# Optimization experiments

Measured on AMD Instinct MI355X. Metric: run time of the kernel, lower is better.

## Reference

```python
import jax, jax.numpy as jnp
import numpy as np

B = 16          # batch
DF = 1536       # dinov2 feature dim
D = 1024        # projected dim (32*32)
V = 6890        # SMPL vertices (hard-coded in DECO)
PD = 256        # vertex positional-embedding dim
HID = 512       # feature_transform hidden dim
C = 133         # semantic contact classes


def setup_inputs() -> dict:
    key = jax.random.key(0)
    ks = jax.random.split(key, 16)
    s = 0.02
    n = lambda k, shp: s * jax.random.normal(k, shp, dtype=jnp.float32)
    return {
        "features": jax.random.normal(ks[0], (B, DF), dtype=jnp.float32),
        "W_scene": n(ks[1], (DF, D)), "b_scene": jnp.zeros((D,), jnp.float32),
        "W_contact": n(ks[2], (DF, D)), "b_contact": jnp.zeros((D,), jnp.float32),
        "Wq": n(ks[3], (D, D)), "Wk": n(ks[4], (D, D)),
        "Wv": n(ks[5], (D, D)), "Wo": n(ks[6], (D, D)),
        "W_cls": n(ks[7], (D, V)), "b_cls": jnp.zeros((V,), jnp.float32),
        "pos_emb": n(ks[8], (V, PD)),
        "W_ft1": n(ks[9], (D + PD, HID)), "b_ft1": jnp.zeros((HID,), jnp.float32),
        "W_ft2": n(ks[10], (HID, C)), "b_ft2": jnp.zeros((C,), jnp.float32),
    }


def reference(features, W_scene, b_scene, W_contact, b_contact,
              Wq, Wk, Wv, Wo, W_cls, b_cls, pos_emb,
              W_ft1, b_ft1, W_ft2, b_ft2):
    b = features.shape[0]
    # projectors (dinov2 branch)
    sem = features @ W_scene + b_scene          # [B, D]
    part = features @ W_contact + b_contact     # [B, D]
    # cross attention over seq-len-1 tokens: q from sem, k/v from part
    q = (sem @ Wq)[:, None, :]                  # [B, 1, D]
    k = (part @ Wk)[:, None, :]
    v = (part @ Wv)[:, None, :]
    scores = jnp.einsum('bqd,bkd->bqk', q, k) / jnp.sqrt(jnp.float32(D))
    w = jax.nn.softmax(scores, axis=-1)
    att = jnp.einsum('bqk,bkd->bqd', w, v) @ Wo  # [B, 1, D]
    # per-vertex contact probability
    cont = jax.nn.sigmoid(att[:, 0, :] @ W_cls + b_cls)  # [B, V]
    # shared semantic classifier: the torch code loops over batches, does
    # nonzero() on (cont > 0.5), gathers pos embeddings for contact vertices,
    # runs feature_transform, and scatters into zeros(B, C, V). The masked
    # vectorized form below computes identical values.
    mask = cont > 0.5                           # [B, V] (int constant wrt grad)
    att_bv = jnp.broadcast_to(att, (b, V, D))   # att[b] repeated per vertex
    pos_bv = jnp.broadcast_to(pos_emb[None], (b, V, PD))
    combined = jnp.concatenate([att_bv, pos_bv], axis=-1)   # [B, V, D+PD]
    h = jax.nn.relu(combined @ W_ft1 + b_ft1)   # [B, V, HID]
    preds = h @ W_ft2 + b_ft2                   # [B, V, C]
    semantic_cont = jnp.where(mask[:, None, :],
                              jnp.transpose(preds, (0, 2, 1)),
                              jnp.float32(0.0))  # [B, C, V]
    return (cont, semantic_cont)
```

## Files before the change

kernel.cpp:

```cpp
#include <hip/hip_runtime.h>
#include <hip/hip_bf16.h>

#define B_   16
#define DF_  1536
#define D_   1024
#define V_   6890
#define PD_  256
#define HID_ 512
#define C_   133
#define VPAD 6912
#define CPAD 144

typedef short short8 __attribute__((ext_vector_type(8)));
typedef float float4_ __attribute__((ext_vector_type(4)));
typedef unsigned short ushort_t;

#define MFMA16 __builtin_amdgcn_mfma_f32_16x16x32_bf16

__device__ __forceinline__ float b2f(ushort_t u) {
  union { unsigned int i; float f; } x;
  x.i = ((unsigned int)u) << 16;
  return x.f;
}
__device__ __forceinline__ ushort_t f2b(float f) {
  union { float f; unsigned int i; } x;
  x.f = f;
  unsigned int r = (x.i + 0x7fffu + ((x.i >> 16) & 1u)) >> 16;
  return (ushort_t)r;
}
__device__ __forceinline__ unsigned int f22u(float h0, float h1) {
  __hip_bfloat162 hb = __float22bfloat162_rn(make_float2(h0, h1));
  unsigned int u;
  __builtin_memcpy(&u, &hb, sizeof(u));
  return u;
}

__global__ __launch_bounds__(256) void k_gemv_fA(const float* __restrict__ A,
                                                 const float* __restrict__ W,
                                                 const float* __restrict__ bias,
                                                 double* __restrict__ outd,
                                                 float* __restrict__ outf,
                                                 int K, int N) {
  int jl = threadIdx.x & 15, ks = threadIdx.x >> 4;
  int b  = blockIdx.y;
  int j  = blockIdx.x * 16 + jl;
  int klen = K >> 4;
  const float* Ar = A + b * K + ks * klen;
  const float* Wp = W + (size_t)(ks * klen) * N + j;
  double acc = 0.0;
#pragma unroll 8
  for (int kk = 0; kk < klen; ++kk)
    acc += (double)Ar[kk] * (double)Wp[(size_t)kk * N];
  __shared__ double red[16][16];
  red[ks][jl] = acc;
  __syncthreads();
  if (threadIdx.x < 16) {
    int jj = blockIdx.x * 16 + threadIdx.x;
    double s = 0.0;
#pragma unroll
    for (int q = 0; q < 16; ++q) s += red[q][threadIdx.x];
    if (bias) s += (double)bias[jj];
    if (outd) outd[b * N + jj] = s;
    if (outf) outf[b * N + jj] = (float)s;
  }
}

__global__ __launch_bounds__(256) void k_gemv_dA(const double* __restrict__ A,
                                                 const float* __restrict__ W,
                                                 const float* __restrict__ bias,
                                                 double* __restrict__ outd,
                                                 float* __restrict__ outf,
                                                 int K, int N) {
  int jl = threadIdx.x & 15, ks = threadIdx.x >> 4;
  int b  = blockIdx.y;
  int j  = blockIdx.x * 16 + jl;
  int klen = K >> 4;
  const double* Ar = A + b * K + ks * klen;
  const float*  Wp = W + (size_t)(ks * klen) * N + j;
  double acc = 0.0;
#pragma unroll 8
  for (int kk = 0; kk < klen; ++kk)
    acc += Ar[kk] * (double)Wp[(size_t)kk * N];
  __shared__ double red[16][16];
  red[ks][jl] = acc;
  __syncthreads();
  if (threadIdx.x < 16) {
    int jj = blockIdx.x * 16 + threadIdx.x;
    double s = 0.0;
#pragma unroll
    for (int q = 0; q < 16; ++q) s += red[q][threadIdx.x];
    if (bias) s += (double)bias[jj];
    if (outd) outd[b * N + jj] = s;
    if (outf) outf[b * N + jj] = (float)s;
  }
}

__global__ __launch_bounds__(256) void k_cont(const double* __restrict__ att,
                                              const float* __restrict__ Wcls,
                                              const float* __restrict__ bcls,
                                              unsigned char* __restrict__ maskb,
                                              float* __restrict__ out0) {
  int vl = threadIdx.x & 15, ks = threadIdx.x >> 4;
  int v  = blockIdx.x * 16 + vl;
  int vc = v < V_ ? v : V_ - 1;
  double acc[B_];
#pragma unroll
  for (int b = 0; b < B_; ++b) acc[b] = 0.0;
  int k0 = ks * 64;
  for (int kk = 0; kk < 64; ++kk) {
    int k = k0 + kk;
    double w = (double)Wcls[(size_t)k * V_ + vc];
#pragma unroll
    for (int b = 0; b < B_; ++b) acc[b] += att[b * D_ + k] * w;
  }
  __shared__ double red[16][B_][16];
#pragma unroll
  for (int b = 0; b < B_; ++b) red[ks][b][vl] = acc[b];
  __syncthreads();
  int b = threadIdx.x >> 4;
  double s = 0.0;
#pragma unroll
  for (int q = 0; q < 16; ++q) s += red[q][b][vl];
  if (v < V_) {
    s += (double)bcls[v];
    maskb[b * V_ + v] = (s > 0.0) ? 1 : 0;
    out0[b * V_ + v] = (float)(1.0 / (1.0 + exp(-s)));
  }
}

__global__ __launch_bounds__(256) void k_prep(const float* __restrict__ Wft2,
                                              const float* __restrict__ Wft1,
                                              ushort_t* __restrict__ WT,
                                              ushort_t* __restrict__ WbT) {
  int i = blockIdx.x * 256 + threadIdx.x;
  if (i < CPAD * HID_) {
    int c = i >> 9, k = i & (HID_ - 1);
    WT[i] = (c < C_) ? f2b(Wft2[(size_t)k * C_ + c]) : (ushort_t)0;
  } else {
    int j = i - CPAD * HID_;
    if (j < HID_ * PD_) {
      int k = j & (HID_ - 1), pd = j >> 9;
      WbT[(size_t)k * PD_ + pd] = f2b(Wft1[(size_t)(D_ + pd) * HID_ + k]);
    }
  }
}

#define LDSROW 264
__global__ __launch_bounds__(256) void k_pproj(const float* __restrict__ pos,
                                               const ushort_t* __restrict__ WbT,
                                               ushort_t* __restrict__ PP) {
  __shared__ ushort_t sp[64 * LDSROW];
  int v0 = blockIdx.x * 64;
#pragma unroll
  for (int k = 0; k < 16; ++k) {
    int flat4 = k * 256 + threadIdx.x;
    int row = flat4 >> 6, col4 = flat4 & 63;
    int vr = v0 + row; vr = vr < V_ ? vr : V_ - 1;
    float4_ x = *(const float4_*)(pos + (size_t)vr * PD_ + col4 * 4);
    unsigned int* dst = (unsigned int*)&sp[row * LDSROW + col4 * 4];
    dst[0] = f22u(x[0], x[1]);
    dst[1] = f22u(x[2], x[3]);
  }
  __syncthreads();

  int wave = threadIdx.x >> 6, lane = threadIdx.x & 63;
  int q = lane >> 4, l15 = lane & 15;
  int n0 = blockIdx.y * 64;
  float4_ acc[4] = {};
  for (int kt = 0; kt < 8; ++kt) {
    int jb = kt * 32 + q * 8;
    short8 a = *(const short8*)&sp[(wave * 16 + l15) * LDSROW + jb];
#pragma unroll
    for (int nf = 0; nf < 4; ++nf) {
      int n = n0 + nf * 16 + l15;
      short8 bfr = *(const short8*)(WbT + (size_t)n * PD_ + jb);
      acc[nf] = MFMA16(a, bfr, acc[nf], 0, 0, 0);
    }
  }
  int v0w = v0 + wave * 16 + q * 4;
#pragma unroll
  for (int nf = 0; nf < 4; ++nf)
#pragma unroll
    for (int r = 0; r < 4; ++r)
      PP[(size_t)(v0w + r) * HID_ + (n0 + nf * 16 + l15)] = f2b(acc[nf][r]);
}

__global__ __launch_bounds__(256, 2) void k_main(const ushort_t* __restrict__ WT,
                                                 const ushort_t* __restrict__ PP,
                                                 const float* __restrict__ attproj,
                                                 const unsigned char* __restrict__ maskb,
                                                 const float* __restrict__ bft2,
                                                 float* __restrict__ out1) {
  int b0 = blockIdx.y * 2;
  int wave = threadIdx.x >> 6, lane = threadIdx.x & 63;
  int q = lane >> 4, l15 = lane & 15;
  int vbase = blockIdx.x * 128 + wave * 32;

  __shared__ float attp[2][HID_];
  for (int i = threadIdx.x; i < 2 * HID_; i += 256)
    attp[i >> 9][i & (HID_ - 1)] = attproj[(b0 + (i >> 9)) * HID_ + (i & (HID_ - 1))];
  __syncthreads();

  const ushort_t* pbase0 = PP + (size_t)(vbase + l15) * HID_;
  const ushort_t* pbase1 = PP + (size_t)(vbase + 16 + l15) * HID_;

  float4_ acc[2][9][2] = {};
  short8 pcur[2];
  pcur[0] = *(const short8*)(pbase0 + q * 8);
  pcur[1] = *(const short8*)(pbase1 + q * 8);

  for (int kt = 0; kt < 16; ++kt) {
    int kb = kt * 32 + q * 8;
    short8 pnext[2] = {pcur[0], pcur[1]};
    if (kt < 15) {
      pnext[0] = *(const short8*)(pbase0 + kb + 32);
      pnext[1] = *(const short8*)(pbase1 + kb + 32);
    }
    float pf[2][8];
#pragma unroll
    for (int nf = 0; nf < 2; ++nf)
#pragma unroll
      for (int jj = 0; jj < 8; ++jj)
        pf[nf][jj] = b2f((ushort_t)pcur[nf][jj]);
    float af[2][8];
#pragma unroll
    for (int bb = 0; bb < 2; ++bb) {
      float4_ a0 = *(const float4_*)&attp[bb][kb];
      float4_ a1 = *(const float4_*)&attp[bb][kb + 4];
#pragma unroll
      for (int e = 0; e < 4; ++e) { af[bb][e] = a0[e]; af[bb][4 + e] = a1[e]; }
    }
    short8 bfr[2][2];
#pragma unroll
    for (int bb = 0; bb < 2; ++bb)
#pragma unroll
      for (int nf = 0; nf < 2; ++nf) {
        unsigned int uu[4];
#pragma unroll
        for (int jj = 0; jj < 8; jj += 2) {
          float h0 = af[bb][jj]     + pf[nf][jj];
          float h1 = af[bb][jj + 1] + pf[nf][jj + 1];
          h0 = h0 > 0.f ? h0 : 0.f;
          h1 = h1 > 0.f ? h1 : 0.f;
          uu[jj >> 1] = f22u(h0, h1);
        }
        __builtin_memcpy(&bfr[bb][nf], uu, 16);
      }
#pragma unroll
    for (int mt = 0; mt < 9; ++mt) {
      short8 a = *(const short8*)(WT + (size_t)(mt * 16 + l15) * HID_ + kb);
      acc[0][mt][0] = MFMA16(a, bfr[0][0], acc[0][mt][0], 0, 0, 0);
      acc[0][mt][1] = MFMA16(a, bfr[0][1], acc[0][mt][1], 0, 0, 0);
      acc[1][mt][0] = MFMA16(a, bfr[1][0], acc[1][mt][0], 0, 0, 0);
      acc[1][mt][1] = MFMA16(a, bfr[1][1], acc[1][mt][1], 0, 0, 0);
    }
    pcur[0] = pnext[0];
    pcur[1] = pnext[1];
  }

  bool mk[2][2];
  int  nn[2];
#pragma unroll
  for (int nf = 0; nf < 2; ++nf) {
    int n = vbase + nf * 16 + l15;
    nn[nf] = n;
    int ncl = n < V_ ? n : V_ - 1;
    mk[0][nf] = (n < V_) && (maskb[(b0 + 0) * V_ + ncl] != 0);
    mk[1][nf] = (n < V_) && (maskb[(b0 + 1) * V_ + ncl] != 0);
  }
#pragma unroll
  for (int bb = 0; bb < 2; ++bb) {
    float* ob = out1 + (size_t)(b0 + bb) * C_ * V_;
#pragma unroll
    for (int mt = 0; mt < 9; ++mt)
#pragma unroll
      for (int r = 0; r < 4; ++r) {
        int c = mt * 16 + q * 4 + r;
        if (c < C_) {
          float bias = bft2[c];
#pragma unroll
          for (int nf = 0; nf < 2; ++nf)
            if (nn[nf] < V_) {
              float val = mk[bb][nf] ? acc[bb][mt][nf][r] + bias : 0.f;
              ob[(size_t)c * V_ + nn[nf]] = val;
            }
        }
      }
  }
}

extern "C" void kernel_launch(void* const* d_in, const int* in_sizes, int n_in,
                              void* d_out, int out_size, void* d_ws, size_t ws_size,
                              hipStream_t stream) {
  const float* features  = (const float*)d_in[0];
  const float* W_contact = (const float*)d_in[3];
  const float* b_contact = (const float*)d_in[4];
  const float* Wv        = (const float*)d_in[7];
  const float* Wo        = (const float*)d_in[8];
  const float* W_cls     = (const float*)d_in[9];
  const float* b_cls     = (const float*)d_in[10];
  const float* pos_emb   = (const float*)d_in[11];
  const float* W_ft1     = (const float*)d_in[12];
  const float* b_ft1     = (const float*)d_in[13];
  const float* W_ft2     = (const float*)d_in[14];
  const float* b_ft2     = (const float*)d_in[15];

  char* ws = (char*)d_ws;
  double*        part  = (double*)(ws);
  unsigned char* maskb = (unsigned char*)(ws);
  double*        vv    = (double*)(ws + 131072);
  double*        att   = (double*)(ws + 262144);
  float*         attpj = (float*)(ws + 393216);
  ushort_t*      wt    = (ushort_t*)(ws + 425984);
  ushort_t*      wbt   = (ushort_t*)(ws + 573440);
  ushort_t*      pp    = (ushort_t*)(ws + 835584);

  float* out0 = (float*)d_out;
  float* out1 = out0 + (size_t)B_ * V_;

  k_prep<<<800, 256, 0, stream>>>(W_ft2, W_ft1, wt, wbt);
  k_pproj<<<dim3(108, 8), 256, 0, stream>>>(pos_emb, wbt, pp);
  k_gemv_fA<<<dim3(64, 16), 256, 0, stream>>>(features, W_contact, b_contact, part, nullptr, DF_, D_);
  k_gemv_dA<<<dim3(64, 16), 256, 0, stream>>>(part, Wv, nullptr, vv, nullptr, D_, D_);
  k_gemv_dA<<<dim3(64, 16), 256, 0, stream>>>(vv, Wo, nullptr, att, nullptr, D_, D_);
  k_gemv_dA<<<dim3(32, 16), 256, 0, stream>>>(att, W_ft1, b_ft1, nullptr, attpj, D_, HID_);
  k_cont<<<432, 256, 0, stream>>>(att, W_cls, b_cls, maskb, out0);
  k_main<<<dim3(54, 8), 256, 0, stream>>>(wt, pp, attpj, maskb, b_ft2, out1);
}
```

Before: 282.8 us.

## Stage GEMV inputs and classifier weights in LDS, pre-convert pos_emb to bf16

The GEMV kernels now copy the per-batch activation row into shared memory before the weight loop. The main kernel double-buffers the bf16 classifier weight tile in LDS instead of reading it from global memory for each MFMA. The pos_emb-to-bf16 conversion moves into the prep kernel, so k_pproj reads bf16 rows directly from global memory, and an unroll pragma is added to k_cont. This adds a larger prep grid, an extra workspace buffer, and a barrier on every k iteration of the main kernel.

```diff
diff --git a/kernel.cpp b/kernel.cpp
--- a/kernel.cpp
+++ b/kernel.cpp
@@ -41,16 +41,19 @@
                                                  double* __restrict__ outd,
                                                  float* __restrict__ outf,
                                                  int K, int N) {
+  __shared__ double sA[DF_];
+  int b = blockIdx.y;
+  for (int i = threadIdx.x; i < K; i += 256) sA[i] = (double)A[b * K + i];
+  __syncthreads();
   int jl = threadIdx.x & 15, ks = threadIdx.x >> 4;
-  int b  = blockIdx.y;
   int j  = blockIdx.x * 16 + jl;
   int klen = K >> 4;
-  const float* Ar = A + b * K + ks * klen;
-  const float* Wp = W + (size_t)(ks * klen) * N + j;
+  const double* Ar = sA + ks * klen;
+  const float*  Wp = W + (size_t)(ks * klen) * N + j;
   double acc = 0.0;
 #pragma unroll 8
   for (int kk = 0; kk < klen; ++kk)
-    acc += (double)Ar[kk] * (double)Wp[(size_t)kk * N];
+    acc += Ar[kk] * (double)Wp[(size_t)kk * N];
   __shared__ double red[16][16];
   red[ks][jl] = acc;
   __syncthreads();
@@ -71,11 +74,14 @@
                                                  double* __restrict__ outd,
                                                  float* __restrict__ outf,
                                                  int K, int N) {
+  __shared__ double sA[D_];
+  int b = blockIdx.y;
+  for (int i = threadIdx.x; i < K; i += 256) sA[i] = A[b * K + i];
+  __syncthreads();
   int jl = threadIdx.x & 15, ks = threadIdx.x >> 4;
-  int b  = blockIdx.y;
   int j  = blockIdx.x * 16 + jl;
   int klen = K >> 4;
-  const double* Ar = A + b * K + ks * klen;
+  const double* Ar = sA + ks * klen;
   const float*  Wp = W + (size_t)(ks * klen) * N + j;
   double acc = 0.0;
 #pragma unroll 8
@@ -107,6 +113,7 @@
 #pragma unroll
   for (int b = 0; b < B_; ++b) acc[b] = 0.0;
   int k0 = ks * 64;
+#pragma unroll 8
   for (int kk = 0; kk < 64; ++kk) {
     int k = k0 + kk;
     double w = (double)Wcls[(size_t)k * V_ + vc];
@@ -130,46 +137,40 @@
 
 __global__ __launch_bounds__(256) void k_prep(const float* __restrict__ Wft2,
                                               const float* __restrict__ Wft1,
+                                              const float* __restrict__ pos,
                                               ushort_t* __restrict__ WT,
-                                              ushort_t* __restrict__ WbT) {
+                                              ushort_t* __restrict__ WbT,
+                                              ushort_t* __restrict__ PB) {
   int i = blockIdx.x * 256 + threadIdx.x;
   if (i < CPAD * HID_) {
     int c = i >> 9, k = i & (HID_ - 1);
     WT[i] = (c < C_) ? f2b(Wft2[(size_t)k * C_ + c]) : (ushort_t)0;
-  } else {
-    int j = i - CPAD * HID_;
-    if (j < HID_ * PD_) {
-      int k = j & (HID_ - 1), pd = j >> 9;
-      WbT[(size_t)k * PD_ + pd] = f2b(Wft1[(size_t)(D_ + pd) * HID_ + k]);
-    }
-  }
-}
-
-#define LDSROW 264
-__global__ __launch_bounds__(256) void k_pproj(const float* __restrict__ pos,
+    return;
+  }
+  i -= CPAD * HID_;
+  if (i < HID_ * PD_) {
+    int k = i & (HID_ - 1), pd = i >> 9;
+    WbT[(size_t)k * PD_ + pd] = f2b(Wft1[(size_t)(D_ + pd) * HID_ + k]);
+    return;
+  }
+  i -= HID_ * PD_;
+  if (i < V_ * PD_) PB[i] = f2b(pos[i]);
+}
+
+__global__ __launch_bounds__(256) void k_pproj(const ushort_t* __restrict__ PB,
                                                const ushort_t* __restrict__ WbT,
                                                ushort_t* __restrict__ PP) {
-  __shared__ ushort_t sp[64 * LDSROW];
-  int v0 = blockIdx.x * 64;
-#pragma unroll
-  for (int k = 0; k < 16; ++k) {
-    int flat4 = k * 256 + threadIdx.x;
-    int row = flat4 >> 6, col4 = flat4 & 63;
-    int vr = v0 + row; vr = vr < V_ ? vr : V_ - 1;
-    float4_ x = *(const float4_*)(pos + (size_t)vr * PD_ + col4 * 4);
-    unsigned int* dst = (unsigned int*)&sp[row * LDSROW + col4 * 4];
-    dst[0] = f22u(x[0], x[1]);
-    dst[1] = f22u(x[2], x[3]);
-  }
-  __syncthreads();
-
   int wave = threadIdx.x >> 6, lane = threadIdx.x & 63;
   int q = lane >> 4, l15 = lane & 15;
+  int m0 = blockIdx.x * 64 + wave * 16;
   int n0 = blockIdx.y * 64;
+  int vc = m0 + l15; vc = vc < V_ ? vc : V_ - 1;
+  const ushort_t* pb = PB + (size_t)vc * PD_;
   float4_ acc[4] = {};
+#pragma unroll 2
   for (int kt = 0; kt < 8; ++kt) {
     int jb = kt * 32 + q * 8;
-    short8 a = *(const short8*)&sp[(wave * 16 + l15) * LDSROW + jb];
+    short8 a = *(const short8*)(pb + jb);
 #pragma unroll
     for (int nf = 0; nf < 4; ++nf) {
       int n = n0 + nf * 16 + l15;
@@ -177,7 +178,7 @@
       acc[nf] = MFMA16(a, bfr, acc[nf], 0, 0, 0);
     }
   }
-  int v0w = v0 + wave * 16 + q * 4;
+  int v0w = m0 + q * 4;
 #pragma unroll
   for (int nf = 0; nf < 4; ++nf)
 #pragma unroll
@@ -191,26 +192,41 @@
                                                  const unsigned char* __restrict__ maskb,
                                                  const float* __restrict__ bft2,
                                                  float* __restrict__ out1) {
+  __shared__ ushort_t swt[2][CPAD * 32];
+  __shared__ float attp[2][HID_];
   int b0 = blockIdx.y * 2;
   int wave = threadIdx.x >> 6, lane = threadIdx.x & 63;
   int q = lane >> 4, l15 = lane & 15;
   int vbase = blockIdx.x * 128 + wave * 32;
 
-  __shared__ float attp[2][HID_];
   for (int i = threadIdx.x; i < 2 * HID_; i += 256)
     attp[i >> 9][i & (HID_ - 1)] = attproj[(b0 + (i >> 9)) * HID_ + (i & (HID_ - 1))];
-  __syncthreads();
+
+  auto stage = [&](int kt, int buf) {
+#pragma unroll
+    for (int ii = 0; ii < 3; ++ii) {
+      int i = ii * 256 + threadIdx.x;
+      if (i < 576) {
+        int row = i >> 2, seg = i & 3;
+        *(short8*)&swt[buf][row * 32 + seg * 8] =
+            *(const short8*)(WT + (size_t)row * HID_ + kt * 32 + seg * 8);
+      }
+    }
+  };
+  stage(0, 0);
 
   const ushort_t* pbase0 = PP + (size_t)(vbase + l15) * HID_;
   const ushort_t* pbase1 = PP + (size_t)(vbase + 16 + l15) * HID_;
-
-  float4_ acc[2][9][2] = {};
   short8 pcur[2];
   pcur[0] = *(const short8*)(pbase0 + q * 8);
   pcur[1] = *(const short8*)(pbase1 + q * 8);
-
+  __syncthreads();
+
+  float4_ acc[2][9][2] = {};
   for (int kt = 0; kt < 16; ++kt) {
+    int buf = kt & 1;
     int kb = kt * 32 + q * 8;
+    if (kt < 15) stage(kt + 1, buf ^ 1);
     short8 pnext[2] = {pcur[0], pcur[1]};
     if (kt < 15) {
       pnext[0] = *(const short8*)(pbase0 + kb + 32);
@@ -248,7 +264,7 @@
       }
 #pragma unroll
     for (int mt = 0; mt < 9; ++mt) {
-      short8 a = *(const short8*)(WT + (size_t)(mt * 16 + l15) * HID_ + kb);
+      short8 a = *(const short8*)&swt[buf][(mt * 16 + l15) * 32 + q * 8];
       acc[0][mt][0] = MFMA16(a, bfr[0][0], acc[0][mt][0], 0, 0, 0);
       acc[0][mt][1] = MFMA16(a, bfr[0][1], acc[0][mt][1], 0, 0, 0);
       acc[1][mt][0] = MFMA16(a, bfr[1][0], acc[1][mt][0], 0, 0, 0);
@@ -256,6 +272,7 @@
     }
     pcur[0] = pnext[0];
     pcur[1] = pnext[1];
+    __syncthreads();
   }
 
   bool mk[2][2];
@@ -314,12 +331,13 @@
   ushort_t*      wt    = (ushort_t*)(ws + 425984);
   ushort_t*      wbt   = (ushort_t*)(ws + 573440);
   ushort_t*      pp    = (ushort_t*)(ws + 835584);
+  ushort_t*      pb    = (ushort_t*)(ws + 7913472);
 
   float* out0 = (float*)d_out;
   float* out1 = out0 + (size_t)B_ * V_;
 
-  k_prep<<<800, 256, 0, stream>>>(W_ft2, W_ft1, wt, wbt);
-  k_pproj<<<dim3(108, 8), 256, 0, stream>>>(pos_emb, wbt, pp);
+  k_prep<<<7690, 256, 0, stream>>>(W_ft2, W_ft1, pos_emb, wt, wbt, pb);
+  k_pproj<<<dim3(108, 8), 256, 0, stream>>>(pb, wbt, pp);
   k_gemv_fA<<<dim3(64, 16), 256, 0, stream>>>(features, W_contact, b_contact, part, nullptr, DF_, D_);
   k_gemv_dA<<<dim3(64, 16), 256, 0, stream>>>(part, Wv, nullptr, vv, nullptr, D_, D_);
   k_gemv_dA<<<dim3(64, 16), 256, 0, stream>>>(vv, Wo, nullptr, att, nullptr, D_, D_);
```

Result: faster. 268.5 us (-5.1%).
